# Kernel optimization log

Measured on AMD Instinct MI355X. Metric: run time of the kernel, lower is better.

The kernel has to match this reference:

```python
import jax, jax.numpy as jnp
import numpy as np

SXY_BF, SC_BF = 70.0, 12.0
COMPAT_BF, COMPAT_SPATIAL = 4.0, 2.0
SXY_SPATIAL = 6
NUM_ITER = 5
N_OUT = 21


def _gkern_depthwise(std, chans):
    # matches gkern(): sig_sq even -> r = sig_sq - 1, s = 2r+1
    sig_sq = std ** 2
    r = sig_sq if sig_sq % 2 else sig_sq - 1
    s = 2 * r + 1
    yy, xx = np.meshgrid(np.arange(s), np.arange(s), indexing='ij')
    k = np.exp(-(((yy - r) ** 2 + (xx - r) ** 2) / (2.0 * sig_sq)))
    k = k / k.sum()
    # original builds a [C,C,s,s] diagonal kernel == depthwise [C,1,s,s]
    return jnp.asarray(np.broadcast_to(k[None, None], (chans, 1, s, s)).copy(), jnp.float32)


def setup_inputs() -> dict:
    key = jax.random.key(0)
    k1, k2 = jax.random.split(key)
    unary = jax.random.uniform(k1, (2, N_OUT, 64, 64), dtype=jnp.float32)
    ref = jax.random.uniform(k2, (2, 3, 64, 64), dtype=jnp.float32) * 255.0  # RGB image
    gk = _gkern_depthwise(SXY_SPATIAL, N_OUT)
    kstd = jnp.asarray([SXY_BF, SXY_BF, SC_BF, SC_BF, SC_BF], jnp.float32)
    return {"unary": unary, "ref": ref, "gk": gk, "kstd": kstd}


def _crf_forward(unary, ref, gk, kstd):
    N, C, H, W = unary.shape
    P = H * W
    # stacked reference features: [y, x, r, g, b]
    yy, xx = jnp.meshgrid(jnp.arange(H, dtype=jnp.float32),
                          jnp.arange(W, dtype=jnp.float32), indexing='ij')
    grid = jnp.broadcast_to(jnp.stack([yy, xx])[None], (N, 2, H, W))
    stacked = jnp.concatenate([grid, ref], axis=1)  # [N,5,H,W]
    feats = (stacked / kstd[None, :, None, None]).reshape(N, -1, P).transpose(0, 2, 1)  # [N,P,5]
    # exact dense Gaussian (bilateral) kernel: K[p,q] = exp(-||f_p - f_q||^2 / 2)
    sq = jnp.sum(feats * feats, axis=-1)  # [N,P]
    d2 = sq[:, :, None] + sq[:, None, :] - 2.0 * jnp.einsum('npd,nqd->npq', feats, feats)
    K = jnp.exp(-0.5 * jnp.maximum(d2, 0.0))  # [N,P,P]

    U = jnp.log(jnp.clip(unary, 1e-5, 1.0))
    q = jax.nn.softmax(U, axis=1)
    pad = gk.shape[-1] // 2
    for i in range(NUM_ITER):
        qbf = jnp.einsum('npq,ncq->ncp', K, q.reshape(N, C, P)).reshape(N, C, H, W)
        qsf = jax.lax.conv_general_dilated(
            q, gk, window_strides=(1, 1), padding=[(pad, pad), (pad, pad)],
            feature_group_count=C, dimension_numbers=('NCHW', 'OIHW', 'NCHW'))
        q_hat = U + COMPAT_BF * qbf + COMPAT_SPATIAL * qsf
        q = jax.nn.softmax(q_hat, axis=1)  # normalize_final_iter=True
    return q


def reference(unary, ref, gk, kstd):
    return _crf_forward(unary, ref, gk, kstd)
```

## Files before the change

kernel.cpp:

```cpp
#include <hip/hip_runtime.h>
#include <math.h>

#ifndef __has_builtin
#define __has_builtin(x) 0
#endif
#if __has_builtin(__builtin_amdgcn_exp2f)
#define EXP2F(x) __builtin_amdgcn_exp2f(x)
#else
#define EXP2F(x) exp2f(x)
#endif

#define L2E  1.44269504088896340736f
#define RL2E 0.69314718055994530942f

#define NBATCH 2
#define NC 21
#define NP 4096
#define KR 35
#define NUM_ITER 5

typedef _Float16 half_t;
typedef _Float16 h8 __attribute__((ext_vector_type(8)));
typedef _Float16 h4 __attribute__((ext_vector_type(4)));
typedef float f4 __attribute__((ext_vector_type(4)));
typedef float f2 __attribute__((ext_vector_type(2)));
#define MFMA16(a, b, c) __builtin_amdgcn_mfma_f32_16x16x32_f16((a), (b), (c), 0, 0, 0)

static __device__ __forceinline__ f2 pk_fma(f2 a, f2 b, f2 c) {
    f2 d;
    asm volatile("v_pk_fma_f32 %0, %1, %2, %3" : "=v"(d) : "v"(a), "v"(b), "v"(c));
    return d;
}
static __device__ __forceinline__ f2 pk_add(f2 a, f2 b) {
    f2 d;
    asm volatile("v_pk_add_f32 %0, %1, %2" : "=v"(d) : "v"(a), "v"(b));
    return d;
}

#define PTILE 256
#define NPT   16
#define MTW   4
#define SQ    16
#define CHUNK 256
#define STEPS 8
#define NBBIL (NBATCH * NPT * SQ)
#define NBCONV (NBATCH * NC)
#define NBTOT  (NBBIL + NBCONV)
#define SEG_HALVES 256

#define OFF_QFEAT 0
#define OFF_QSOA  65536
#define OFF_UT    114688
#define OFF_QSF   311296
#define OFF_G     483328
#define OFF_QH16  485376
#define OFF_PART  845824

#define LDS_BYTES 27648
#define QLS_STRIDE 264

__global__ __launch_bounds__(256) void setup_kernel(
    const float* __restrict__ unary, const float* __restrict__ ref,
    const float* __restrict__ kstd, float* __restrict__ ws,
    float* __restrict__ outq)
{
    int gid = blockIdx.x * 256 + threadIdx.x;
    if (gid < 4096) {
        float s = 0.f;
        for (int t = -KR; t <= KR; ++t) s += expf(-(float)(t * t) * (1.0f / 72.0f));
        int y = gid >> 6, yp = gid & 63;
        int d = y - yp;
        float v = (d >= -KR && d <= KR) ? expf(-(float)(d * d) * (1.0f / 72.0f)) / s : 0.f;
        ((half_t*)(ws + OFF_G))[gid] = (half_t)v;
    }
    if (gid >= NBATCH * NP) return;
    int n = gid >> 12, p = gid & (NP - 1);
    int y = p >> 6, x = p & 63;
    float k0 = kstd[0], k1 = kstd[1], k2 = kstd[2], k3 = kstd[3], k4 = kstd[4];
    const float* rp = ref + n * 3 * NP + p;
    float f0 = (float)y / k0;
    float f1 = (float)x / k1;
    float f2_ = rp[0]      / k2;
    float f3 = rp[NP]     / k3;
    float f4_ = rp[2 * NP] / k4;
    float sq = f0*f0 + f1*f1 + f2_*f2_ + f3*f3 + f4_*f4_;
    float h  = -0.5f * L2E * sq;
    float* qf = ws + OFF_QFEAT + gid * 8;
    qf[0]=L2E*f0; qf[1]=L2E*f1; qf[2]=L2E*f2_; qf[3]=L2E*f3; qf[4]=L2E*f4_;
    qf[5]=h; qf[6]=0.f; qf[7]=0.f;
    float* qs = ws + OFF_QSOA;
    qs[0*8192 + gid] = L2E*f0;  qs[1*8192 + gid] = L2E*f1;
    qs[2*8192 + gid] = L2E*f2_; qs[3*8192 + gid] = L2E*f3;
    qs[4*8192 + gid] = L2E*f4_; qs[5*8192 + gid] = h;

    float U[NC], e[NC];
    const float* up = unary + n * NC * NP + p;
    float m = -1e30f;
    for (int c = 0; c < NC; ++c) {
        float u = up[c * NP];
        u = fminf(fmaxf(u, 1e-5f), 1.0f);
        U[c] = logf(u);
        m = fmaxf(m, U[c]);
    }
    float ssum = 0.f;
    for (int c = 0; c < NC; ++c) { e[c] = EXP2F(L2E * (U[c] - m)); ssum += e[c]; }
    float inv = 1.0f / ssum;
    float* ut = ws + OFF_UT + gid * 24;
    half_t* qh = (half_t*)(ws + OFF_QH16);
    for (int c = 0; c < NC; ++c) {
        float qv = e[c] * inv;
        ut[c] = U[c];
        qh[(n * 24 + c) * NP + p] = (half_t)qv;
        outq[(n * NC + c) * NP + p] = qv;
    }
    ut[21] = 0.f; ut[22] = 0.f; ut[23] = 0.f;
    qh[(n * 24 + 21) * NP + p] = (half_t)0.f;
    qh[(n * 24 + 22) * NP + p] = (half_t)0.f;
    qh[(n * 24 + 23) * NP + p] = (half_t)0.f;
}

__global__ __launch_bounds__(256) void bilat_conv_kernel(
    const float* __restrict__ qfeatA,
    const float* __restrict__ qsoa,
    const half_t* __restrict__ qh16,
    const half_t* __restrict__ gmat,
    half_t* __restrict__ part,
    float* __restrict__ qsf)
{
    __shared__ __align__(16) char lds[LDS_BYTES];
    int b = blockIdx.x;
    int tid = threadIdx.x;
    int l = tid & 63, w = tid >> 6;

    if (b < NBBIL) {
        int n  = b & 1;
        int pt = (b >> 1) & (NPT - 1);
        int s  = b >> 5;
        float*  qsoaS = (float*)lds;
        half_t* qls   = (half_t*)(lds + 6144);

        for (int i = tid; i < 6 * (CHUNK / 4); i += 256) {
            int d = i >> 6, g = i & 63;
            *(f4*)(qsoaS + d * CHUNK + g * 4) =
                *(const f4*)(qsoa + (size_t)d * 8192 + n * NP + s * CHUNK + g * 4);
        }
        for (int i = tid; i < 21 * (CHUNK / 8); i += 256) {
            int c = i >> 5, g = i & 31;
            *(h8*)(qls + c * QLS_STRIDE + g * 8) =
                *(const h8*)(qh16 + (size_t)(n * 24 + c) * NP + s * CHUNK + g * 8);
        }
        for (int i = tid; i < 11 * 33; i += 256) {
            int c = 21 + i / 33, g = i % 33;
            *(h8*)(qls + c * QLS_STRIDE + g * 8) = (h8)(half_t)0.f;
        }
        f2 pf2[MTW][5], ph2[MTW];
        #pragma unroll
        for (int mt = 0; mt < MTW; ++mt) {
            const float* fp = qfeatA + (size_t)(n * NP + pt * PTILE + (w * MTW + mt) * 16 + (l & 15)) * 8;
            #pragma unroll
            for (int i = 0; i < 5; ++i) {
                float v = fp[i] * RL2E;
                pf2[mt][i] = (f2){v, v};
            }
            ph2[mt] = (f2){fp[5], fp[5]};
        }
        f4 acc[MTW][2];
        #pragma unroll
        for (int mt = 0; mt < MTW; ++mt) { acc[mt][0] = (f4)0.f; acc[mt][1] = (f4)0.f; }
        int kq = (l >> 4) * 8;
        __syncthreads();

        for (int step = 0; step < STEPS; ++step) {
            int qbase = step * 32 + kq;
            h8 kv[MTW];
            #pragma unroll
            for (int hf = 0; hf < 2; ++hf) {
                f4 qf0 = *(const f4*)(qsoaS + 0 * CHUNK + qbase + hf * 4);
                f4 qf1 = *(const f4*)(qsoaS + 1 * CHUNK + qbase + hf * 4);
                f4 qf2 = *(const f4*)(qsoaS + 2 * CHUNK + qbase + hf * 4);
                f4 qf3 = *(const f4*)(qsoaS + 3 * CHUNK + qbase + hf * 4);
                f4 qf4 = *(const f4*)(qsoaS + 4 * CHUNK + qbase + hf * 4);
                f4 qf5 = *(const f4*)(qsoaS + 5 * CHUNK + qbase + hf * 4);
                #pragma unroll
                for (int pr = 0; pr < 2; ++pr) {
                    f2 q0 = {qf0[2*pr], qf0[2*pr+1]};
                    f2 q1 = {qf1[2*pr], qf1[2*pr+1]};
                    f2 q2 = {qf2[2*pr], qf2[2*pr+1]};
                    f2 q3 = {qf3[2*pr], qf3[2*pr+1]};
                    f2 q4 = {qf4[2*pr], qf4[2*pr+1]};
                    f2 qh2 = {qf5[2*pr], qf5[2*pr+1]};
                    #pragma unroll
                    for (int mt = 0; mt < MTW; ++mt) {
                        f2 e = pk_add(qh2, ph2[mt]);
                        e = pk_fma(pf2[mt][0], q0, e);
                        e = pk_fma(pf2[mt][1], q1, e);
                        e = pk_fma(pf2[mt][2], q2, e);
                        e = pk_fma(pf2[mt][3], q3, e);
                        e = pk_fma(pf2[mt][4], q4, e);
                        kv[mt][hf * 4 + pr * 2]     = (half_t)EXP2F(e[0]);
                        kv[mt][hf * 4 + pr * 2 + 1] = (half_t)EXP2F(e[1]);
                    }
                }
            }
            h8 bf0 = *(const h8*)(qls + (size_t)(l & 15) * QLS_STRIDE + qbase);
            h8 bf1 = *(const h8*)(qls + (size_t)(16 + (l & 15)) * QLS_STRIDE + qbase);
            #pragma unroll
            for (int mt = 0; mt < MTW; ++mt) {
                acc[mt][0] = MFMA16(kv[mt], bf0, acc[mt][0]);
                acc[mt][1] = MFMA16(kv[mt], bf1, acc[mt][1]);
            }
        }
        #pragma unroll
        for (int mt = 0; mt < MTW; ++mt) {
            #pragma unroll
            for (int cht = 0; cht < 2; ++cht) {
                int segFlat = ((((s * 2 + n) * NPT + pt) * 4 + w) * MTW + mt) * 2 + cht;
                h4 hv;
                hv[0] = (half_t)acc[mt][cht][0];
                hv[1] = (half_t)acc[mt][cht][1];
                hv[2] = (half_t)acc[mt][cht][2];
                hv[3] = (half_t)acc[mt][cht][3];
                *(h4*)(part + (size_t)segFlat * SEG_HALVES + l * 4) = hv;
            }
        }
    } else {
        int cb = b - NBBIL;
        int n = cb / NC, c = cb % NC;
        half_t* qt = (half_t*)lds;
        half_t* gl = (half_t*)(lds + 9216);
        half_t* dl = (half_t*)(lds + 18432);

        for (int i = tid; i < 512; i += 256) {
            int row = i >> 3, g = i & 7;
            *(h8*)(gl + row * 72 + g * 8) = *(const h8*)(gmat + row * 64 + g * 8);
        }
        const half_t* qsrc = qh16 + (size_t)(n * 24 + c) * NP;
        for (int i = tid; i < 512; i += 256) {
            int row = i >> 3, g = i & 7;
            h8 v = *(const h8*)(qsrc + row * 64 + g * 8);
            #pragma unroll
            for (int k = 0; k < 8; ++k) qt[(g * 8 + k) * 72 + row] = v[k];
        }
        __syncthreads();

        int m0 = w * 16;
        f4 acc1[4];
        #pragma unroll
        for (int nt = 0; nt < 4; ++nt) acc1[nt] = (f4)0.f;
        #pragma unroll
        for (int ks = 0; ks < 2; ++ks) {
            h8 af = *(const h8*)(gl + (size_t)(m0 + (l & 15)) * 72 + ks * 32 + (l >> 4) * 8);
            #pragma unroll
            for (int nt = 0; nt < 4; ++nt) {
                h8 bf = *(const h8*)(qt + (size_t)(nt * 16 + (l & 15)) * 72 + ks * 32 + (l >> 4) * 8);
                acc1[nt] = MFMA16(af, bf, acc1[nt]);
            }
        }
        #pragma unroll
        for (int nt = 0; nt < 4; ++nt)
            #pragma unroll
            for (int r = 0; r < 4; ++r)
                dl[(size_t)(m0 + (l >> 4) * 4 + r) * 72 + nt * 16 + (l & 15)] = (half_t)acc1[nt][r];
        __syncthreads();

        f4 acc2[4];
        #pragma unroll
        for (int nt = 0; nt < 4; ++nt) acc2[nt] = (f4)0.f;
        #pragma unroll
        for (int ks = 0; ks < 2; ++ks) {
            h8 af = *(const h8*)(dl + (size_t)(m0 + (l & 15)) * 72 + ks * 32 + (l >> 4) * 8);
            #pragma unroll
            for (int nt = 0; nt < 4; ++nt) {
                h8 bf = *(const h8*)(gl + (size_t)(nt * 16 + (l & 15)) * 72 + ks * 32 + (l >> 4) * 8);
                acc2[nt] = MFMA16(af, bf, acc2[nt]);
            }
        }
        float* dst = qsf + (size_t)(n * NC + c) * NP;
        #pragma unroll
        for (int nt = 0; nt < 4; ++nt)
            #pragma unroll
            for (int r = 0; r < 4; ++r)
                dst[(size_t)(m0 + (l >> 4) * 4 + r) * 64 + nt * 16 + (l & 15)] = acc2[nt][r];
    }
}

__global__ __launch_bounds__(256) void reduce_update_kernel(
    const half_t* __restrict__ part, const float* __restrict__ ut_,
    const float* __restrict__ qsf, float* __restrict__ outq,
    half_t* __restrict__ qh16, int last)
{
    __shared__ float red[1024];
    int rb = blockIdx.x;
    int tid = threadIdx.x;
    int n = rb & 1, pt = (rb >> 1) & (NPT - 1), wq = rb >> 5;
    int w = wq >> 1, mtbase = (wq & 1) * 2;
    int lseg = tid >> 6, l = tid & 63;

    const half_t* pb = part
        + (size_t)(n * 512 + pt * 32 + w * 8 + mtbase * 2 + lseg) * SEG_HALVES
        + (size_t)l * 4;
    h4 vv[16];
    #pragma unroll
    for (int s = 0; s < SQ; ++s)
        vv[s] = *(const h4*)(pb + (size_t)s * 1024 * SEG_HALVES);

    float a0 = 0.f, a1 = 0.f, a2 = 0.f, a3 = 0.f;
    #pragma unroll
    for (int s = 0; s < SQ; ++s) {
        a0 += (float)vv[s][0]; a1 += (float)vv[s][1];
        a2 += (float)vv[s][2]; a3 += (float)vv[s][3];
    }
    *(f4*)(red + tid * 4) = (f4){a0, a1, a2, a3};
    __syncthreads();

    if (tid < 32) {
        int pp = tid;
        int p = pt * PTILE + wq * 32 + pp;
        int gid = n * NP + p;
        int mtl = pp >> 4, mrow = pp & 15;
        int lg2 = mrow >> 2, reg = mrow & 3;

        const float* ut = ut_ + (size_t)gid * 24;
        const float* qs = qsf + (size_t)n * NC * NP + p;
        float e[NC];
        float m = -1e30f;
        #pragma unroll
        for (int c = 0; c < NC; ++c) {
            int cht = c >> 4, chL = c & 15;
            float qb = red[(mtl * 2 + cht) * 256 + (lg2 * 16 + chL) * 4 + reg];
            float li = ut[c] + 4.0f * qb + 2.0f * qs[c * NP];
            e[c] = li;
            m = fmaxf(m, li);
        }
        float ssum = 0.f;
        #pragma unroll
        for (int c = 0; c < NC; ++c) { float v = EXP2F(L2E * (e[c] - m)); e[c] = v; ssum += v; }
        float inv = 1.0f / ssum;
        if (last) {
            #pragma unroll
            for (int c = 0; c < NC; ++c)
                outq[(size_t)(n * NC + c) * NP + p] = e[c] * inv;
        } else {
            #pragma unroll
            for (int c = 0; c < NC; ++c)
                qh16[(size_t)(n * 24 + c) * NP + p] = (half_t)(e[c] * inv);
        }
    }
}

extern "C" void kernel_launch(void* const* d_in, const int* in_sizes, int n_in,
                              void* d_out, int out_size, void* d_ws, size_t ws_size,
                              hipStream_t stream)
{
    const float* unary = (const float*)d_in[0];
    const float* ref   = (const float*)d_in[1];
    const float* kstd  = (const float*)d_in[3];
    float* ws   = (float*)d_ws;
    float* outq = (float*)d_out;

    const float*  qfeatA = ws + OFF_QFEAT;
    const float*  qsoa   = ws + OFF_QSOA;
    float*        ut     = ws + OFF_UT;
    float*        qsf    = ws + OFF_QSF;
    const half_t* gmat   = (const half_t*)(ws + OFF_G);
    half_t*       qh16   = (half_t*)(ws + OFF_QH16);
    half_t*       part   = (half_t*)(ws + OFF_PART);

    setup_kernel<<<32, 256, 0, stream>>>(unary, ref, kstd, ws, outq);
    for (int it = 0; it < NUM_ITER; ++it) {
        bilat_conv_kernel<<<NBTOT, 256, 0, stream>>>(
            qfeatA, qsoa, qh16, gmat, part, qsf);
        reduce_update_kernel<<<256, 256, 0, stream>>>(
            part, ut, qsf, outq, qh16, it == NUM_ITER - 1 ? 1 : 0);
    }
}
```

Before: 144.5 us.

## Remove setup kernel by recomputing features, softmax and Gaussian in main kernels

Drops the separate setup launch and its workspace tensors. Bilateral blocks derive pixel features directly from the reference image and, in the first iteration, compute the initial softmax from the unary input. Conv blocks rebuild the 1D Gaussian matrix each launch and recompute the per-channel initial softmax, and the update kernel recomputes log(unary) each iteration. This saves one launch and workspace traffic, at the cost of substantial redundant transcendental work, especially in the first-iteration conv blocks.

```diff
diff --git a/kernel.cpp b/kernel.cpp
--- a/kernel.cpp
+++ b/kernel.cpp
@@ -48,106 +48,77 @@
 #define NBTOT  (NBBIL + NBCONV)
 #define SEG_HALVES 256
 
-#define OFF_QFEAT 0
-#define OFF_QSOA  65536
-#define OFF_UT    114688
 #define OFF_QSF   311296
-#define OFF_G     483328
 #define OFF_QH16  485376
 #define OFF_PART  845824
 
 #define LDS_BYTES 27648
 #define QLS_STRIDE 264
 
-__global__ __launch_bounds__(256) void setup_kernel(
-    const float* __restrict__ unary, const float* __restrict__ ref,
-    const float* __restrict__ kstd, float* __restrict__ ws,
-    float* __restrict__ outq)
-{
-    int gid = blockIdx.x * 256 + threadIdx.x;
-    if (gid < 4096) {
-        float s = 0.f;
-        for (int t = -KR; t <= KR; ++t) s += expf(-(float)(t * t) * (1.0f / 72.0f));
-        int y = gid >> 6, yp = gid & 63;
-        int d = y - yp;
-        float v = (d >= -KR && d <= KR) ? expf(-(float)(d * d) * (1.0f / 72.0f)) / s : 0.f;
-        ((half_t*)(ws + OFF_G))[gid] = (half_t)v;
-    }
-    if (gid >= NBATCH * NP) return;
-    int n = gid >> 12, p = gid & (NP - 1);
-    int y = p >> 6, x = p & 63;
-    float k0 = kstd[0], k1 = kstd[1], k2 = kstd[2], k3 = kstd[3], k4 = kstd[4];
-    const float* rp = ref + n * 3 * NP + p;
-    float f0 = (float)y / k0;
-    float f1 = (float)x / k1;
-    float f2_ = rp[0]      / k2;
-    float f3 = rp[NP]     / k3;
-    float f4_ = rp[2 * NP] / k4;
-    float sq = f0*f0 + f1*f1 + f2_*f2_ + f3*f3 + f4_*f4_;
-    float h  = -0.5f * L2E * sq;
-    float* qf = ws + OFF_QFEAT + gid * 8;
-    qf[0]=L2E*f0; qf[1]=L2E*f1; qf[2]=L2E*f2_; qf[3]=L2E*f3; qf[4]=L2E*f4_;
-    qf[5]=h; qf[6]=0.f; qf[7]=0.f;
-    float* qs = ws + OFF_QSOA;
-    qs[0*8192 + gid] = L2E*f0;  qs[1*8192 + gid] = L2E*f1;
-    qs[2*8192 + gid] = L2E*f2_; qs[3*8192 + gid] = L2E*f3;
-    qs[4*8192 + gid] = L2E*f4_; qs[5*8192 + gid] = h;
-
-    float U[NC], e[NC];
-    const float* up = unary + n * NC * NP + p;
-    float m = -1e30f;
-    for (int c = 0; c < NC; ++c) {
-        float u = up[c * NP];
-        u = fminf(fmaxf(u, 1e-5f), 1.0f);
-        U[c] = logf(u);
-        m = fmaxf(m, U[c]);
-    }
-    float ssum = 0.f;
-    for (int c = 0; c < NC; ++c) { e[c] = EXP2F(L2E * (U[c] - m)); ssum += e[c]; }
-    float inv = 1.0f / ssum;
-    float* ut = ws + OFF_UT + gid * 24;
-    half_t* qh = (half_t*)(ws + OFF_QH16);
-    for (int c = 0; c < NC; ++c) {
-        float qv = e[c] * inv;
-        ut[c] = U[c];
-        qh[(n * 24 + c) * NP + p] = (half_t)qv;
-        outq[(n * NC + c) * NP + p] = qv;
-    }
-    ut[21] = 0.f; ut[22] = 0.f; ut[23] = 0.f;
-    qh[(n * 24 + 21) * NP + p] = (half_t)0.f;
-    qh[(n * 24 + 22) * NP + p] = (half_t)0.f;
-    qh[(n * 24 + 23) * NP + p] = (half_t)0.f;
-}
-
 __global__ __launch_bounds__(256) void bilat_conv_kernel(
-    const float* __restrict__ qfeatA,
-    const float* __restrict__ qsoa,
+    const float* __restrict__ unary,
+    const float* __restrict__ ref,
+    const float* __restrict__ kstd,
     const half_t* __restrict__ qh16,
-    const half_t* __restrict__ gmat,
     half_t* __restrict__ part,
-    float* __restrict__ qsf)
+    float* __restrict__ qsf,
+    int first)
 {
     __shared__ __align__(16) char lds[LDS_BYTES];
     int b = blockIdx.x;
     int tid = threadIdx.x;
     int l = tid & 63, w = tid >> 6;
 
-    if (b < NBBIL) {
-        int n  = b & 1;
-        int pt = (b >> 1) & (NPT - 1);
-        int s  = b >> 5;
+    if (b >= NBCONV) {
+        int bb = b - NBCONV;
+        int n  = bb & 1;
+        int pt = (bb >> 1) & (NPT - 1);
+        int s  = bb >> 5;
         float*  qsoaS = (float*)lds;
         half_t* qls   = (half_t*)(lds + 6144);
 
-        for (int i = tid; i < 6 * (CHUNK / 4); i += 256) {
-            int d = i >> 6, g = i & 63;
-            *(f4*)(qsoaS + d * CHUNK + g * 4) =
-                *(const f4*)(qsoa + (size_t)d * 8192 + n * NP + s * CHUNK + g * 4);
-        }
-        for (int i = tid; i < 21 * (CHUNK / 8); i += 256) {
-            int c = i >> 5, g = i & 31;
-            *(h8*)(qls + c * QLS_STRIDE + g * 8) =
-                *(const h8*)(qh16 + (size_t)(n * 24 + c) * NP + s * CHUNK + g * 8);
+        float k0 = kstd[0], k1 = kstd[1], k2 = kstd[2], k3 = kstd[3], k4 = kstd[4];
+
+        {
+            int pq = s * CHUNK + tid;
+            int y = pq >> 6, x = pq & 63;
+            const float* rp = ref + n * 3 * NP + pq;
+            float f0 = (float)y / k0;
+            float f1 = (float)x / k1;
+            float f2_ = rp[0]      / k2;
+            float f3 = rp[NP]     / k3;
+            float f4_ = rp[2 * NP] / k4;
+            float sq = f0*f0 + f1*f1 + f2_*f2_ + f3*f3 + f4_*f4_;
+            float h  = -0.5f * L2E * sq;
+            qsoaS[0 * CHUNK + tid] = L2E * f0;
+            qsoaS[1 * CHUNK + tid] = L2E * f1;
+            qsoaS[2 * CHUNK + tid] = L2E * f2_;
+            qsoaS[3 * CHUNK + tid] = L2E * f3;
+            qsoaS[4 * CHUNK + tid] = L2E * f4_;
+            qsoaS[5 * CHUNK + tid] = h;
+        }
+        if (first) {
+            int pg = s * CHUNK + tid;
+            const float* up = unary + (size_t)n * NC * NP + pg;
+            float U[NC], e[NC];
+            float m = -1e30f;
+            for (int cc = 0; cc < NC; ++cc) {
+                float u = up[cc * NP];
+                u = fminf(fmaxf(u, 1e-5f), 1.0f);
+                U[cc] = logf(u);
+                m = fmaxf(m, U[cc]);
+            }
+            float ssum = 0.f;
+            for (int cc = 0; cc < NC; ++cc) { e[cc] = EXP2F(L2E * (U[cc] - m)); ssum += e[cc]; }
+            float inv = 1.0f / ssum;
+            for (int cc = 0; cc < NC; ++cc)
+                qls[cc * QLS_STRIDE + tid] = (half_t)(e[cc] * inv);
+        } else {
+            for (int i = tid; i < 21 * (CHUNK / 8); i += 256) {
+                int c = i >> 5, g = i & 31;
+                *(h8*)(qls + c * QLS_STRIDE + g * 8) =
+                    *(const h8*)(qh16 + (size_t)(n * 24 + c) * NP + s * CHUNK + g * 8);
+            }
         }
         for (int i = tid; i < 11 * 33; i += 256) {
             int c = 21 + i / 33, g = i % 33;
@@ -156,13 +127,24 @@
         f2 pf2[MTW][5], ph2[MTW];
         #pragma unroll
         for (int mt = 0; mt < MTW; ++mt) {
-            const float* fp = qfeatA + (size_t)(n * NP + pt * PTILE + (w * MTW + mt) * 16 + (l & 15)) * 8;
+            int pp = pt * PTILE + (w * MTW + mt) * 16 + (l & 15);
+            int y = pp >> 6, x = pp & 63;
+            const float* rp = ref + n * 3 * NP + pp;
+            float f[5];
+            f[0] = (float)y / k0;
+            f[1] = (float)x / k1;
+            f[2] = rp[0]      / k2;
+            f[3] = rp[NP]     / k3;
+            f[4] = rp[2 * NP] / k4;
+            float sq = f[0]*f[0] + f[1]*f[1] + f[2]*f[2] + f[3]*f[3] + f[4]*f[4];
+            float h  = -0.5f * L2E * sq;
             #pragma unroll
             for (int i = 0; i < 5; ++i) {
-                float v = fp[i] * RL2E;
+                float qfv = L2E * f[i];
+                float v = qfv * RL2E;
                 pf2[mt][i] = (f2){v, v};
             }
-            ph2[mt] = (f2){fp[5], fp[5]};
+            ph2[mt] = (f2){h, h};
         }
         f4 acc[MTW][2];
         #pragma unroll
@@ -224,22 +206,60 @@
             }
         }
     } else {
-        int cb = b - NBBIL;
-        int n = cb / NC, c = cb % NC;
+        int n = b / NC, c = b % NC;
         half_t* qt = (half_t*)lds;
         half_t* gl = (half_t*)(lds + 9216);
         half_t* dl = (half_t*)(lds + 18432);
 
-        for (int i = tid; i < 512; i += 256) {
-            int row = i >> 3, g = i & 7;
-            *(h8*)(gl + row * 72 + g * 8) = *(const h8*)(gmat + row * 64 + g * 8);
-        }
-        const half_t* qsrc = qh16 + (size_t)(n * 24 + c) * NP;
-        for (int i = tid; i < 512; i += 256) {
-            int row = i >> 3, g = i & 7;
-            h8 v = *(const h8*)(qsrc + row * 64 + g * 8);
-            #pragma unroll
-            for (int k = 0; k < 8; ++k) qt[(g * 8 + k) * 72 + row] = v[k];
+        {
+            float s71 = 0.f;
+            for (int t = -KR; t <= KR; ++t) s71 += expf(-(float)(t * t) * (1.0f / 72.0f));
+            for (int i = tid; i < 512; i += 256) {
+                int row = i >> 3, g = i & 7;
+                h8 v;
+                #pragma unroll
+                for (int k = 0; k < 8; ++k) {
+                    int col = g * 8 + k;
+                    int d = row - col;
+                    float vv = (d >= -KR && d <= KR)
+                        ? expf(-(float)(d * d) * (1.0f / 72.0f)) / s71 : 0.f;
+                    v[k] = (half_t)vv;
+                }
+                *(h8*)(gl + row * 72 + g * 8) = v;
+            }
+        }
+        if (first) {
+            for (int i = tid; i < 512; i += 256) {
+                int row = i >> 3, g = i & 7;
+                for (int k = 0; k < 8; ++k) {
+                    int p = row * 64 + g * 8 + k;
+                    const float* up = unary + (size_t)n * NC * NP + p;
+                    float U[NC];
+                    float m = -1e30f;
+                    for (int cc = 0; cc < NC; ++cc) {
+                        float u = up[cc * NP];
+                        u = fminf(fmaxf(u, 1e-5f), 1.0f);
+                        U[cc] = logf(u);
+                        m = fmaxf(m, U[cc]);
+                    }
+                    float ssum = 0.f, ec = 0.f;
+                    for (int cc = 0; cc < NC; ++cc) {
+                        float e = EXP2F(L2E * (U[cc] - m));
+                        ssum += e;
+                        if (cc == c) ec = e;
+                    }
+                    float inv = 1.0f / ssum;
+                    qt[(g * 8 + k) * 72 + row] = (half_t)(ec * inv);
+                }
+            }
+        } else {
+            const half_t* qsrc = qh16 + (size_t)(n * 24 + c) * NP;
+            for (int i = tid; i < 512; i += 256) {
+                int row = i >> 3, g = i & 7;
+                h8 v = *(const h8*)(qsrc + row * 64 + g * 8);
+                #pragma unroll
+                for (int k = 0; k < 8; ++k) qt[(g * 8 + k) * 72 + row] = v[k];
+            }
         }
         __syncthreads();
 
@@ -285,7 +305,7 @@
 }
 
 __global__ __launch_bounds__(256) void reduce_update_kernel(
-    const half_t* __restrict__ part, const float* __restrict__ ut_,
+    const half_t* __restrict__ part, const float* __restrict__ unary,
     const float* __restrict__ qsf, float* __restrict__ outq,
     half_t* __restrict__ qh16, int last)
 {
@@ -316,19 +336,21 @@
     if (tid < 32) {
         int pp = tid;
         int p = pt * PTILE + wq * 32 + pp;
-        int gid = n * NP + p;
         int mtl = pp >> 4, mrow = pp & 15;
         int lg2 = mrow >> 2, reg = mrow & 3;
 
-        const float* ut = ut_ + (size_t)gid * 24;
+        const float* up = unary + (size_t)n * NC * NP + p;
         const float* qs = qsf + (size_t)n * NC * NP + p;
         float e[NC];
         float m = -1e30f;
         #pragma unroll
         for (int c = 0; c < NC; ++c) {
+            float u = up[c * NP];
+            u = fminf(fmaxf(u, 1e-5f), 1.0f);
+            float U = logf(u);
             int cht = c >> 4, chL = c & 15;
             float qb = red[(mtl * 2 + cht) * 256 + (lg2 * 16 + chL) * 4 + reg];
-            float li = ut[c] + 4.0f * qb + 2.0f * qs[c * NP];
+            float li = U + 4.0f * qb + 2.0f * qs[c * NP];
             e[c] = li;
             m = fmaxf(m, li);
         }
@@ -358,19 +380,14 @@
     float* ws   = (float*)d_ws;
     float* outq = (float*)d_out;
 
-    const float*  qfeatA = ws + OFF_QFEAT;
-    const float*  qsoa   = ws + OFF_QSOA;
-    float*        ut     = ws + OFF_UT;
-    float*        qsf    = ws + OFF_QSF;
-    const half_t* gmat   = (const half_t*)(ws + OFF_G);
-    half_t*       qh16   = (half_t*)(ws + OFF_QH16);
-    half_t*       part   = (half_t*)(ws + OFF_PART);
-
-    setup_kernel<<<32, 256, 0, stream>>>(unary, ref, kstd, ws, outq);
+    float*  qsf  = ws + OFF_QSF;
+    half_t* qh16 = (half_t*)(ws + OFF_QH16);
+    half_t* part = (half_t*)(ws + OFF_PART);
+
     for (int it = 0; it < NUM_ITER; ++it) {
         bilat_conv_kernel<<<NBTOT, 256, 0, stream>>>(
-            qfeatA, qsoa, qh16, gmat, part, qsf);
+            unary, ref, kstd, qh16, part, qsf, it == 0 ? 1 : 0);
         reduce_update_kernel<<<256, 256, 0, stream>>>(
-            part, ut, qsf, outq, qh16, it == NUM_ITER - 1 ? 1 : 0);
+            part, unary, qsf, outq, qh16, it == NUM_ITER - 1 ? 1 : 0);
     }
 }
```

After: 206.7 us. +43.1%, slower.
